# Performance work log

Hardware: AMD Instinct MI355X
Metric: run time of the kernel (lower is better)

The kernel has to match this reference:

```python
import jax, jax.numpy as jnp
import numpy as np
import math

M = 8                      # multiplicity (channels per irrep)
COMBOS = [(0,0,0),(0,1,1),(1,0,1),(1,1,0),(1,1,1),(2,1,1)]  # (edge_l, node_l, out_l)

def _cg_coeff(j1, m1, j2, m2, j3, m3):
    # standard (Racah) complex Clebsch-Gordan coefficient <j1 m1 j2 m2 | j3 m3>
    if m3 != m1 + m2:
        return 0.0
    f = math.factorial
    vmin = max(0, j2 - j3 - m1, j1 + m2 - j3)
    vmax = min(j1 + j2 - j3, j1 - m1, j2 + m2)
    pref = (2*j3 + 1) * f(j3+j1-j2) * f(j3-j1+j2) * f(j1+j2-j3) / f(j1+j2+j3+1)
    pref *= f(j3+m3) * f(j3-m3) * f(j1-m1) * f(j1+m1) * f(j2-m2) * f(j2+m2)
    s = 0.0
    for v in range(vmin, vmax + 1):
        s += (-1)**v / (f(v) * f(j1+j2-j3-v) * f(j1-m1-v) * f(j2+m2-v)
                        * f(j3-j2+m1+v) * f(j3-j1-m2+v))
    return math.sqrt(pref) * s

def _su2_cg(l1, l2, l3):
    C = np.zeros((2*l1+1, 2*l2+1, 2*l3+1), dtype=np.complex128)
    for m1 in range(-l1, l1+1):
        for m2 in range(-l2, l2+1):
            m3 = m1 + m2
            if -l3 <= m3 <= l3:
                C[m1+l1, m2+l2, m3+l3] = _cg_coeff(l1, m1, l2, m2, l3, m3)
    return C

def _qmat(l):
    # real -> complex spherical-harmonic change of basis (e3nn convention)
    q = np.zeros((2*l+1, 2*l+1), dtype=np.complex128)
    for m in range(-l, 0):
        q[l+m, l+abs(m)] = 1/np.sqrt(2)
        q[l+m, l-abs(m)] = -1j/np.sqrt(2)
    q[l, l] = 1.0
    for m in range(1, l+1):
        q[l+m, l+abs(m)] = (-1)**m / np.sqrt(2)
        q[l+m, l-abs(m)] = 1j * (-1)**m / np.sqrt(2)
    return (-1j)**l * q

def _so3_cg(l1, l2, l3):
    # real-basis CG, normalized to unit Frobenius norm (matches e3nn _so3_clebsch_gordan)
    C = np.einsum('ij,kl,mn,ikn->jlm', _qmat(l1), _qmat(l2),
                  np.conj(_qmat(l3)).T, _su2_cg(l1, l2, l3))
    assert np.abs(C.imag).max() < 1e-6
    C = C.real
    return C / np.linalg.norm(C)

CG = {c: jnp.asarray(_so3_cg(*c), dtype=jnp.float32) for c in COMBOS}


def setup_inputs() -> dict:
    N, E = 100000, 1600000
    ks = jax.random.split(jax.random.key(0), 6)
    return {
        'node_irreps': jax.random.normal(ks[0], (N, 4*M), jnp.float32),
        'edge_index': jax.random.randint(ks[1], (2, E), 0, N, dtype=jnp.int32),
        'sh0': jax.random.normal(ks[2], (E, 1), jnp.float32),
        'sh1': jax.random.normal(ks[3], (E, 3), jnp.float32),
        'sh2': jax.random.normal(ks[4], (E, 5), jnp.float32),
        'W': jax.random.normal(ks[5], (len(COMBOS), M, M), jnp.float32),
    }


def reference(node_irreps, edge_index, sh0, sh1, sh2, W):
    N, E = node_irreps.shape[0], edge_index.shape[1]
    src = node_irreps[edge_index[0]]                    # gather: [E, 4M]
    feats = {0: src[:, :M][:, :, None],                 # scalar channels [E, M, 1]
             1: src[:, M:].reshape(E, M, 3)}            # vector channels [E, M, 3]
    sh = {0: sh0, 1: sh1, 2: sh2}
    msg = {0: jnp.zeros((E, M, 1), node_irreps.dtype),
           1: jnp.zeros((E, M, 3), node_irreps.dtype)}
    for idx, (le, ln, lo) in enumerate(COMBOS):
        # per-edge CG tensor product: [de,dn,do] x [E,de] x [E,M,dn] -> [E,M,do]
        base = jnp.einsum('ijk,ei,emj->emk', CG[(le, ln, lo)], sh[le], feats[ln])
        # channel-mixing scalar weights (in_channel -> out_channel)
        msg[lo] = msg[lo] + jnp.einsum('io,eik->eok', W[idx], base)
    tgt = edge_index[1]
    agg0 = jax.ops.segment_sum(msg[0].reshape(E, M), tgt, num_segments=N)     # [N, M]
    agg1 = jax.ops.segment_sum(msg[1].reshape(E, 3*M), tgt, num_segments=N)   # [N, 3M]
    return jnp.concatenate([agg0, agg1], axis=1)
```

## Files before the change

kernel.cpp:

```cpp
#include <hip/hip_runtime.h>

#define THREADS 256

typedef float v4f __attribute__((ext_vector_type(4)));


__global__ __launch_bounds__(THREADS) void k_hist(const int* __restrict__ tgt,
                                                  int* __restrict__ cnt, int E) {
    int e = blockIdx.x * THREADS + threadIdx.x;
    if (e < E) atomicAdd(&cnt[tgt[e]], 1);
}

__global__ __launch_bounds__(THREADS) void k_scan_partial(const int* __restrict__ cnt,
                                                          int* __restrict__ bsum, int N) {
    __shared__ int lds[THREADS];
    int base = blockIdx.x * 1024 + threadIdx.x * 4;
    int s = 0;
    #pragma unroll
    for (int k = 0; k < 4; ++k) { int i = base + k; if (i < N) s += cnt[i]; }
    lds[threadIdx.x] = s; __syncthreads();
    for (int off = THREADS / 2; off > 0; off >>= 1) {
        if (threadIdx.x < off) lds[threadIdx.x] += lds[threadIdx.x + off];
        __syncthreads();
    }
    if (threadIdx.x == 0) bsum[blockIdx.x] = lds[0];
}

__global__ __launch_bounds__(1024) void k_scan_bsum(int* __restrict__ bsum, int NB) {
    __shared__ int lds[1024];
    int t = threadIdx.x;
    int v = (t < NB) ? bsum[t] : 0;
    lds[t] = v; __syncthreads();
    for (int off = 1; off < 1024; off <<= 1) {
        int x = (t >= off) ? lds[t - off] : 0;
        __syncthreads();
        lds[t] += x;
        __syncthreads();
    }
    if (t < NB) bsum[t] = lds[t] - v;
}

__global__ __launch_bounds__(THREADS) void k_scan_final(int* __restrict__ cnt,
                                                        const int* __restrict__ bsum,
                                                        int* __restrict__ rowptr,
                                                        int N, int E) {
    __shared__ int lds[THREADS];
    int base = blockIdx.x * 1024 + threadIdx.x * 4;
    int v[4]; int local = 0;
    #pragma unroll
    for (int k = 0; k < 4; ++k) {
        int i = base + k;
        v[k] = (i < N) ? cnt[i] : 0;
        local += v[k];
    }
    lds[threadIdx.x] = local; __syncthreads();
    for (int off = 1; off < THREADS; off <<= 1) {
        int x = (threadIdx.x >= off) ? lds[threadIdx.x - off] : 0;
        __syncthreads();
        lds[threadIdx.x] += x;
        __syncthreads();
    }
    int p = lds[threadIdx.x] - local + bsum[blockIdx.x];
    #pragma unroll
    for (int k = 0; k < 4; ++k) {
        int i = base + k;
        if (i < N) { rowptr[i] = p; cnt[i] = p; p += v[k]; }
    }
    if (blockIdx.x == 0 && threadIdx.x == 0) rowptr[N] = E;
}


__global__ __launch_bounds__(THREADS) void k_scatter3(const int* __restrict__ eidx,
                                                      int* __restrict__ cursor,
                                                      const float* __restrict__ sh0,
                                                      const float* __restrict__ sh1,
                                                      const float* __restrict__ sh2,
                                                      float* __restrict__ pay,
                                                      int E) {
    int e = blockIdx.x * THREADS + threadIdx.x;
    if (e >= E) return;

    constexpr float IS10 = 0.31622776601683794f;
    constexpr float IS30 = 0.18257418583505536f;

    const int src = eidx[e];
    const int tgt = eidx[E + e];
    const int pos = atomicAdd(&cursor[tgt], 1);

    const float s  = __builtin_nontemporal_load(&sh0[e]);
    const float u0 = __builtin_nontemporal_load(&sh1[3*e+0]);
    const float u1 = __builtin_nontemporal_load(&sh1[3*e+1]);
    const float u2 = __builtin_nontemporal_load(&sh1[3*e+2]);
    const float q0 = __builtin_nontemporal_load(&sh2[5*e+0]);
    const float q1 = __builtin_nontemporal_load(&sh2[5*e+1]);
    const float q2 = __builtin_nontemporal_load(&sh2[5*e+2]);
    const float q3 = __builtin_nontemporal_load(&sh2[5*e+3]);
    const float q4 = __builtin_nontemporal_load(&sh2[5*e+4]);

    const float Q00 = -q2*IS30 - q4*IS10;
    const float Q01 =  q1*IS10;
    const float Q02 =  q0*IS10;
    const float Q11 =  2.0f*q2*IS30;
    const float Q12 =  q3*IS10;
    const float Q22 = -q2*IS30 + q4*IS10;

    float4* pr = (float4*)(pay + (size_t)pos * 16);
    pr[0] = make_float4(s, u0, u1, u2);
    pr[1] = make_float4(Q00, Q01, Q02, Q11);
    pr[2] = make_float4(Q12, Q22, __int_as_float(src), 0.f);
    pr[3] = make_float4(0.f, 0.f, 0.f, 0.f);
}


#define ACC_STRIDE 15

__global__ __launch_bounds__(THREADS) void k_agg6(const float* __restrict__ node,
                                                  const int*   __restrict__ rowptr,
                                                  const float* __restrict__ pay,
                                                  const float* __restrict__ W,
                                                  float*       __restrict__ out, int N) {
    __shared__ float sW[384];
    __shared__ float sAcc[32 * 8 * ACC_STRIDE];
    for (int t = threadIdx.x; t < 384; t += THREADS) sW[t] = W[t];
    __syncthreads();

    constexpr float IS3  = 0.57735026918962576f;
    constexpr float IS6  = 0.40824829046386302f;

    const int nodeSlot = threadIdx.x >> 3;
    const int i        = threadIdx.x & 7;
    const int n        = blockIdx.x * 32 + nodeSlot;

    float a[14];
    #pragma unroll
    for (int k = 0; k < 14; ++k) a[k] = 0.f;

    if (n < N) {
        const int jbeg = rowptr[n];
        const int jend = rowptr[n + 1];

        if (jbeg < jend) {
            const int jlast = jend - 1;

            const v4f* p0 = (const v4f*)(pay + (size_t)jbeg * 16);
            v4f c0 = __builtin_nontemporal_load(p0 + 0);
            v4f c1 = __builtin_nontemporal_load(p0 + 1);
            v4f c2 = __builtin_nontemporal_load(p0 + 2);
            const int s0 = __float_as_int(c2[2]);
            const float* nr0 = node + (size_t)s0 * 32;
            float f0 = nr0[i];
            float x  = nr0[8 + 3*i + 0];
            float y  = nr0[8 + 3*i + 1];
            float z  = nr0[8 + 3*i + 2];

            const int j1 = (jbeg + 1 < jend) ? jbeg + 1 : jlast;
            const v4f* p1 = (const v4f*)(pay + (size_t)j1 * 16);
            v4f d0 = __builtin_nontemporal_load(p1 + 0);
            v4f d1 = __builtin_nontemporal_load(p1 + 1);
            v4f d2 = __builtin_nontemporal_load(p1 + 2);

            for (int j = jbeg; j < jend; ++j) {
                const int sn = __float_as_int(d2[2]);
                const float* nrn = node + (size_t)sn * 32;
                const float nf0 = nrn[i];
                const float nx  = nrn[8 + 3*i + 0];
                const float ny  = nrn[8 + 3*i + 1];
                const float nz  = nrn[8 + 3*i + 2];
                const int j2 = (j + 2 < jend) ? j + 2 : jlast;
                const v4f* p2 = (const v4f*)(pay + (size_t)j2 * 16);
                const v4f e0 = __builtin_nontemporal_load(p2 + 0);
                const v4f e1 = __builtin_nontemporal_load(p2 + 1);
                const v4f e2 = __builtin_nontemporal_load(p2 + 2);

                const float s  = c0[0], u0 = c0[1], u1 = c0[2], u2 = c0[3];
                const float Q00 = c1[0], Q01 = c1[1], Q02 = c1[2], Q11 = c1[3];
                const float Q12 = c2[0], Q22 = c2[1];

                a[0]  += s * f0;
                a[1]  += u0*x + u1*y + u2*z;
                a[2]  += s * x;
                a[3]  += s * y;
                a[4]  += s * z;
                a[5]  += f0 * u0;
                a[6]  += f0 * u1;
                a[7]  += f0 * u2;
                a[8]  += u1*z - u2*y;
                a[9]  += u2*x - u0*z;
                a[10] += u0*y - u1*x;
                a[11] += Q00*x + Q01*y + Q02*z;
                a[12] += Q01*x + Q11*y + Q12*z;
                a[13] += Q02*x + Q12*y + Q22*z;

                c0 = d0; c1 = d1; c2 = d2;
                d0 = e0; d1 = e1; d2 = e2;
                f0 = nf0; x = nx; y = ny; z = nz;
            }
        }
    }

    #pragma unroll
    for (int k = 1; k < 8; ++k) a[k] *= IS3;
    #pragma unroll
    for (int k = 8; k < 11; ++k) a[k] *= IS6;

    float* myAcc = &sAcc[(nodeSlot * 8 + i) * ACC_STRIDE];
    #pragma unroll
    for (int k = 0; k < 14; ++k) myAcc[k] = a[k];
    __syncthreads();

    if (n < N) {
        const int o = i;
        float o0 = 0.f, ox = 0.f, oy = 0.f, oz = 0.f;
        #pragma unroll
        for (int ii = 0; ii < 8; ++ii) {
            const float* A = &sAcc[(nodeSlot * 8 + ii) * ACC_STRIDE];
            const float w0 = sW[  0 + ii*8 + o];
            const float w1 = sW[ 64 + ii*8 + o];
            const float w2 = sW[128 + ii*8 + o];
            const float w3 = sW[192 + ii*8 + o];
            const float w4 = sW[256 + ii*8 + o];
            const float w5 = sW[320 + ii*8 + o];
            o0 += w0*A[0]  + w3*A[1];
            ox += w1*A[2]  + w2*A[5] + w4*A[8]  + w5*A[11];
            oy += w1*A[3]  + w2*A[6] + w4*A[9]  + w5*A[12];
            oz += w1*A[4]  + w2*A[7] + w4*A[10] + w5*A[13];
        }
        float* orow = out + (size_t)n * 32;
        orow[o]         = o0;
        orow[8 + 3*o+0] = ox;
        orow[8 + 3*o+1] = oy;
        orow[8 + 3*o+2] = oz;
    }
}


__global__ __launch_bounds__(THREADS) void msg_kernel_atomic(
    const float* __restrict__ node,
    const int*   __restrict__ eidx,
    const float* __restrict__ sh0,
    const float* __restrict__ sh1,
    const float* __restrict__ sh2,
    const float* __restrict__ W,
    float*       __restrict__ out,
    int E)
{
    __shared__ float sW[384];
    for (int t = threadIdx.x; t < 384; t += THREADS) sW[t] = W[t];
    __syncthreads();

    int e = blockIdx.x * THREADS + threadIdx.x;
    if (e >= E) return;

    constexpr float IS3  = 0.57735026918962576f;
    constexpr float IS6  = 0.40824829046386302f;
    constexpr float IS10 = 0.31622776601683794f;
    constexpr float IS30 = 0.18257418583505536f;

    const int src = eidx[e];
    const int tgt = eidx[E + e];

    const float s  = sh0[e];
    const float u0 = sh1[3*e+0], u1 = sh1[3*e+1], u2 = sh1[3*e+2];
    const float q0 = sh2[5*e+0], q1 = sh2[5*e+1], q2 = sh2[5*e+2],
                q3 = sh2[5*e+3], q4 = sh2[5*e+4];

    const float Q00 = -q2*IS30 - q4*IS10;
    const float Q01 =  q1*IS10;
    const float Q02 =  q0*IS10;
    const float Q11 =  2.0f*q2*IS30;
    const float Q12 =  q3*IS10;
    const float Q22 = -q2*IS30 + q4*IS10;

    float f[32];
    {
        const float4* nr = (const float4*)(node + (size_t)src * 32);
        #pragma unroll
        for (int i = 0; i < 8; ++i) {
            float4 v = nr[i];
            f[4*i+0]=v.x; f[4*i+1]=v.y; f[4*i+2]=v.z; f[4*i+3]=v.w;
        }
    }

    float msg[32];
    #pragma unroll
    for (int j = 0; j < 32; ++j) msg[j] = 0.0f;

    const float s13 = s * IS3;

    #pragma unroll
    for (int i = 0; i < 8; ++i) {
        const float f0i = f[i];
        const float x = f[8+3*i+0], y = f[8+3*i+1], z = f[8+3*i+2];
        const float c0  = s * f0i;
        const float c3  = IS3 * (u0*x + u1*y + u2*z);
        const float p2  = IS3 * f0i;
        const float c1x = s13*x, c1y = s13*y, c1z = s13*z;
        const float c2x = p2*u0, c2y = p2*u1, c2z = p2*u2;
        const float c4x = IS6*(u1*z - u2*y);
        const float c4y = IS6*(u2*x - u0*z);
        const float c4z = IS6*(u0*y - u1*x);
        const float c5x = Q00*x + Q01*y + Q02*z;
        const float c5y = Q01*x + Q11*y + Q12*z;
        const float c5z = Q02*x + Q12*y + Q22*z;

        float wr[6][8];
        #pragma unroll
        for (int c = 0; c < 6; ++c) {
            float4 aa = *(const float4*)&sW[c*64 + i*8 + 0];
            float4 bb = *(const float4*)&sW[c*64 + i*8 + 4];
            wr[c][0]=aa.x; wr[c][1]=aa.y; wr[c][2]=aa.z; wr[c][3]=aa.w;
            wr[c][4]=bb.x; wr[c][5]=bb.y; wr[c][6]=bb.z; wr[c][7]=bb.w;
        }

        #pragma unroll
        for (int o = 0; o < 8; ++o) {
            msg[o] += wr[0][o]*c0 + wr[3][o]*c3;
            msg[8+3*o+0] += wr[1][o]*c1x + wr[2][o]*c2x + wr[4][o]*c4x + wr[5][o]*c5x;
            msg[8+3*o+1] += wr[1][o]*c1y + wr[2][o]*c2y + wr[4][o]*c4y + wr[5][o]*c5y;
            msg[8+3*o+2] += wr[1][o]*c1z + wr[2][o]*c2z + wr[4][o]*c4z + wr[5][o]*c5z;
        }
    }

    float* orow = out + (size_t)tgt * 32;
    #pragma unroll
    for (int j = 0; j < 32; ++j) unsafeAtomicAdd(orow + j, msg[j]);
}


extern "C" void kernel_launch(void* const* d_in, const int* in_sizes, int n_in,
                              void* d_out, int out_size, void* d_ws, size_t ws_size,
                              hipStream_t stream) {
    const float* node = (const float*)d_in[0];
    const int*   eidx = (const int*)d_in[1];
    const float* sh0  = (const float*)d_in[2];
    const float* sh1  = (const float*)d_in[3];
    const float* sh2  = (const float*)d_in[4];
    const float* W    = (const float*)d_in[5];
    float* out = (float*)d_out;

    const int E = in_sizes[2];
    const int N = in_sizes[0] / 32;
    const int NB = (N + 1023) / 1024;

    size_t int_words = (size_t)(N + 1) + N + 1024;
    size_t pay_off_w = (int_words + 15) & ~(size_t)15;
    size_t need      = (pay_off_w + (size_t)E * 16) * sizeof(float);

    const int gridE = (E + THREADS - 1) / THREADS;

    if (ws_size >= need && NB <= 1024) {
        int* rowptr = (int*)d_ws;
        int* cnt    = rowptr + (N + 1);
        int* bsum   = cnt + N;
        float* pay  = (float*)d_ws + pay_off_w;

        hipMemsetAsync(cnt, 0, (size_t)N * sizeof(int), stream);

        k_hist<<<gridE, THREADS, 0, stream>>>(eidx + E, cnt, E);
        k_scan_partial<<<NB, THREADS, 0, stream>>>(cnt, bsum, N);
        k_scan_bsum<<<1, 1024, 0, stream>>>(bsum, NB);
        k_scan_final<<<NB, THREADS, 0, stream>>>(cnt, bsum, rowptr, N, E);

        k_scatter3<<<gridE, THREADS, 0, stream>>>(eidx, cnt, sh0, sh1, sh2, pay, E);

        k_agg6<<<(N + 31) / 32, THREADS, 0, stream>>>(node, rowptr, pay, W, out, N);
    } else {
        hipMemsetAsync(d_out, 0, (size_t)out_size * sizeof(float), stream);
        msg_kernel_atomic<<<gridE, THREADS, 0, stream>>>(
            node, eidx, sh0, sh1, sh2, W, out, E);
    }
}
```

Measured before the change: 360.8 us.

## Parallelize edges across lanes in aggregation, precompute edge ranks, transpose node features

The aggregation kernel now gives each wavefront 8 nodes processed one at a time. Within a node, the 8 lane groups each take a different edge of a chunk of 8, and the partial sums are reduced with cross-lane shuffles. Before, each thread walked a node's whole edge list serially. The histogram pass now records each edge's rank within its target, so the scatter pass computes the CSR position directly instead of doing a second atomic. A new transpose kernel repacks node features so each lane's (scalar, x, y, z) is one contiguous 16-byte load. These add workspace use and an extra kernel, plus shuffle reduction work per node.

Result: slower. 375.1 us (+3.9%).

```diff
diff --git a/kernel.cpp b/kernel.cpp
--- a/kernel.cpp
+++ b/kernel.cpp
@@ -4,6 +4,13 @@
 
 typedef float v4f __attribute__((ext_vector_type(4)));
 
+
+__global__ __launch_bounds__(THREADS) void k_hist2(const int* __restrict__ tgt,
+                                                   int* __restrict__ cnt,
+                                                   int* __restrict__ ke, int E) {
+    int e = blockIdx.x * THREADS + threadIdx.x;
+    if (e < E) ke[e] = atomicAdd(&cnt[tgt[e]], 1);
+}
 
 __global__ __launch_bounds__(THREADS) void k_hist(const int* __restrict__ tgt,
                                                   int* __restrict__ cnt, int E) {
@@ -70,7 +77,24 @@
 }
 
 
-__global__ __launch_bounds__(THREADS) void k_scatter3(const int* __restrict__ eidx,
+__global__ __launch_bounds__(THREADS) void k_ntrans(const float* __restrict__ node,
+                                                    float* __restrict__ nodeT, int NT8) {
+    int t = blockIdx.x * THREADS + threadIdx.x;
+    if (t >= NT8) return;
+    int n = t >> 3, i = t & 7;
+    const float* nr = node + (size_t)n * 32;
+    v4f v;
+    v[0] = nr[i];
+    v[1] = nr[8 + 3*i + 0];
+    v[2] = nr[8 + 3*i + 1];
+    v[3] = nr[8 + 3*i + 2];
+    *(v4f*)(nodeT + (size_t)t * 4) = v;
+}
+
+
+__global__ __launch_bounds__(THREADS) void k_scatter4(const int* __restrict__ eidx,
+                                                      const int* __restrict__ ke,
+                                                      const int* __restrict__ rowptr,
                                                       int* __restrict__ cursor,
                                                       const float* __restrict__ sh0,
                                                       const float* __restrict__ sh1,
@@ -85,7 +109,9 @@
 
     const int src = eidx[e];
     const int tgt = eidx[E + e];
-    const int pos = atomicAdd(&cursor[tgt], 1);
+    int pos;
+    if (ke) pos = rowptr[tgt] + ke[e];
+    else    pos = atomicAdd(&cursor[tgt], 1);
 
     const float s  = __builtin_nontemporal_load(&sh0[e]);
     const float u0 = __builtin_nontemporal_load(&sh1[3*e+0]);
@@ -114,122 +140,155 @@
 
 #define ACC_STRIDE 15
 
-__global__ __launch_bounds__(THREADS) void k_agg6(const float* __restrict__ node,
+__global__ __launch_bounds__(THREADS) void k_agg7(const float* __restrict__ node,
+                                                  const float* __restrict__ nodeT,
                                                   const int*   __restrict__ rowptr,
                                                   const float* __restrict__ pay,
                                                   const float* __restrict__ W,
-                                                  float*       __restrict__ out, int N) {
+                                                  float*       __restrict__ out,
+                                                  int N, int useT) {
     __shared__ float sW[384];
     __shared__ float sAcc[32 * 8 * ACC_STRIDE];
     for (int t = threadIdx.x; t < 384; t += THREADS) sW[t] = W[t];
     __syncthreads();
 
-    constexpr float IS3  = 0.57735026918962576f;
-    constexpr float IS6  = 0.40824829046386302f;
-
-    const int nodeSlot = threadIdx.x >> 3;
-    const int i        = threadIdx.x & 7;
-    const int n        = blockIdx.x * 32 + nodeSlot;
-
-    float a[14];
-    #pragma unroll
-    for (int k = 0; k < 14; ++k) a[k] = 0.f;
-
-    if (n < N) {
-        const int jbeg = rowptr[n];
-        const int jend = rowptr[n + 1];
-
-        if (jbeg < jend) {
-            const int jlast = jend - 1;
-
-            const v4f* p0 = (const v4f*)(pay + (size_t)jbeg * 16);
-            v4f c0 = __builtin_nontemporal_load(p0 + 0);
-            v4f c1 = __builtin_nontemporal_load(p0 + 1);
-            v4f c2 = __builtin_nontemporal_load(p0 + 2);
-            const int s0 = __float_as_int(c2[2]);
-            const float* nr0 = node + (size_t)s0 * 32;
-            float f0 = nr0[i];
-            float x  = nr0[8 + 3*i + 0];
-            float y  = nr0[8 + 3*i + 1];
-            float z  = nr0[8 + 3*i + 2];
-
-            const int j1 = (jbeg + 1 < jend) ? jbeg + 1 : jlast;
-            const v4f* p1 = (const v4f*)(pay + (size_t)j1 * 16);
-            v4f d0 = __builtin_nontemporal_load(p1 + 0);
-            v4f d1 = __builtin_nontemporal_load(p1 + 1);
-            v4f d2 = __builtin_nontemporal_load(p1 + 2);
-
-            for (int j = jbeg; j < jend; ++j) {
-                const int sn = __float_as_int(d2[2]);
-                const float* nrn = node + (size_t)sn * 32;
-                const float nf0 = nrn[i];
-                const float nx  = nrn[8 + 3*i + 0];
-                const float ny  = nrn[8 + 3*i + 1];
-                const float nz  = nrn[8 + 3*i + 2];
-                const int j2 = (j + 2 < jend) ? j + 2 : jlast;
-                const v4f* p2 = (const v4f*)(pay + (size_t)j2 * 16);
-                const v4f e0 = __builtin_nontemporal_load(p2 + 0);
-                const v4f e1 = __builtin_nontemporal_load(p2 + 1);
-                const v4f e2 = __builtin_nontemporal_load(p2 + 2);
-
-                const float s  = c0[0], u0 = c0[1], u1 = c0[2], u2 = c0[3];
-                const float Q00 = c1[0], Q01 = c1[1], Q02 = c1[2], Q11 = c1[3];
-                const float Q12 = c2[0], Q22 = c2[1];
-
-                a[0]  += s * f0;
-                a[1]  += u0*x + u1*y + u2*z;
-                a[2]  += s * x;
-                a[3]  += s * y;
-                a[4]  += s * z;
-                a[5]  += f0 * u0;
-                a[6]  += f0 * u1;
-                a[7]  += f0 * u2;
-                a[8]  += u1*z - u2*y;
-                a[9]  += u2*x - u0*z;
-                a[10] += u0*y - u1*x;
-                a[11] += Q00*x + Q01*y + Q02*z;
-                a[12] += Q01*x + Q11*y + Q12*z;
-                a[13] += Q02*x + Q12*y + Q22*z;
-
-                c0 = d0; c1 = d1; c2 = d2;
-                d0 = e0; d1 = e1; d2 = e2;
-                f0 = nf0; x = nx; y = ny; z = nz;
+    constexpr float IS3 = 0.57735026918962576f;
+    constexpr float IS6 = 0.40824829046386302f;
+
+    const int lane  = threadIdx.x & 63;
+    const int wv    = threadIdx.x >> 6;
+    const int i     = lane & 7;
+    const int jslot = lane >> 3;
+    const int nbase = blockIdx.x * 32 + wv * 8;
+
+    for (int t = 0; t < 8; ++t) {
+        const int n = nbase + t;
+
+        float a[14];
+        #pragma unroll
+        for (int k = 0; k < 14; ++k) a[k] = 0.f;
+
+        if (n < N) {
+            const int jbeg = rowptr[n];
+            const int jend = rowptr[n + 1];
+
+            if (jbeg < jend) {
+                int j  = jbeg + jslot;
+                int jc = (j < jend) ? j : (jend - 1);
+                float mcur = (j < jend) ? 1.f : 0.f;
+                const v4f* p = (const v4f*)(pay + (size_t)jc * 16);
+                v4f c0 = p[0], c1 = p[1], c2 = p[2];
+                int src = __float_as_int(c2[2]);
+                v4f nf;
+                if (useT) {
+                    nf = *(const v4f*)(nodeT + ((size_t)src * 8 + i) * 4);
+                } else {
+                    const float* nr = node + (size_t)src * 32;
+                    nf[0] = nr[i];
+                    nf[1] = nr[8 + 3*i + 0];
+                    nf[2] = nr[8 + 3*i + 1];
+                    nf[3] = nr[8 + 3*i + 2];
+                }
+
+                for (int g0 = jbeg; g0 < jend; g0 += 8) {
+                    const int gn = g0 + 8;
+                    const bool more = gn < jend;
+                    v4f d0, d1, d2; float mnext = 0.f;
+                    if (more) {
+                        int jn  = gn + jslot;
+                        int jnc = (jn < jend) ? jn : (jend - 1);
+                        mnext = (jn < jend) ? 1.f : 0.f;
+                        const v4f* pn = (const v4f*)(pay + (size_t)jnc * 16);
+                        d0 = pn[0]; d1 = pn[1]; d2 = pn[2];
+                    }
+
+                    const float f0 = nf[0] * mcur;
+                    const float x  = nf[1] * mcur;
+                    const float y  = nf[2] * mcur;
+                    const float z  = nf[3] * mcur;
+                    const float s   = c0[0], u0 = c0[1], u1 = c0[2], u2 = c0[3];
+                    const float Q00 = c1[0], Q01 = c1[1], Q02 = c1[2], Q11 = c1[3];
+                    const float Q12 = c2[0], Q22 = c2[1];
+
+                    a[0]  += s * f0;
+                    a[1]  += u0*x + u1*y + u2*z;
+                    a[2]  += s * x;
+                    a[3]  += s * y;
+                    a[4]  += s * z;
+                    a[5]  += f0 * u0;
+                    a[6]  += f0 * u1;
+                    a[7]  += f0 * u2;
+                    a[8]  += u1*z - u2*y;
+                    a[9]  += u2*x - u0*z;
+                    a[10] += u0*y - u1*x;
+                    a[11] += Q00*x + Q01*y + Q02*z;
+                    a[12] += Q01*x + Q11*y + Q12*z;
+                    a[13] += Q02*x + Q12*y + Q22*z;
+
+                    if (more) {
+                        int srcn = __float_as_int(d2[2]);
+                        if (useT) {
+                            nf = *(const v4f*)(nodeT + ((size_t)srcn * 8 + i) * 4);
+                        } else {
+                            const float* nrn = node + (size_t)srcn * 32;
+                            nf[0] = nrn[i];
+                            nf[1] = nrn[8 + 3*i + 0];
+                            nf[2] = nrn[8 + 3*i + 1];
+                            nf[3] = nrn[8 + 3*i + 2];
+                        }
+                        c0 = d0; c1 = d1; c2 = d2; mcur = mnext;
+                    }
+                }
             }
         }
-    }
-
-    #pragma unroll
-    for (int k = 1; k < 8; ++k) a[k] *= IS3;
-    #pragma unroll
-    for (int k = 8; k < 11; ++k) a[k] *= IS6;
-
-    float* myAcc = &sAcc[(nodeSlot * 8 + i) * ACC_STRIDE];
-    #pragma unroll
-    for (int k = 0; k < 14; ++k) myAcc[k] = a[k];
+
+        #pragma unroll
+        for (int k = 0; k < 14; ++k) {
+            float v = a[k];
+            v += __shfl_xor(v, 8);
+            v += __shfl_xor(v, 16);
+            v += __shfl_xor(v, 32);
+            a[k] = v;
+        }
+
+        if (n < N && jslot == 0) {
+            #pragma unroll
+            for (int k = 1; k < 8; ++k) a[k] *= IS3;
+            #pragma unroll
+            for (int k = 8; k < 11; ++k) a[k] *= IS6;
+            float* myAcc = &sAcc[((wv * 8 + t) * 8 + i) * ACC_STRIDE];
+            #pragma unroll
+            for (int k = 0; k < 14; ++k) myAcc[k] = a[k];
+        }
+    }
     __syncthreads();
 
-    if (n < N) {
-        const int o = i;
-        float o0 = 0.f, ox = 0.f, oy = 0.f, oz = 0.f;
-        #pragma unroll
-        for (int ii = 0; ii < 8; ++ii) {
-            const float* A = &sAcc[(nodeSlot * 8 + ii) * ACC_STRIDE];
-            const float w0 = sW[  0 + ii*8 + o];
-            const float w1 = sW[ 64 + ii*8 + o];
-            const float w2 = sW[128 + ii*8 + o];
-            const float w3 = sW[192 + ii*8 + o];
-            const float w4 = sW[256 + ii*8 + o];
-            const float w5 = sW[320 + ii*8 + o];
-            o0 += w0*A[0]  + w3*A[1];
-            ox += w1*A[2]  + w2*A[5] + w4*A[8]  + w5*A[11];
-            oy += w1*A[3]  + w2*A[6] + w4*A[9]  + w5*A[12];
-            oz += w1*A[4]  + w2*A[7] + w4*A[10] + w5*A[13];
-        }
-        float* orow = out + (size_t)n * 32;
-        orow[o]         = o0;
-        orow[8 + 3*o+0] = ox;
-        orow[8 + 3*o+1] = oy;
-        orow[8 + 3*o+2] = oz;
+    {
+        const int nodeSlot = threadIdx.x >> 3;
+        const int o        = threadIdx.x & 7;
+        const int n        = blockIdx.x * 32 + nodeSlot;
+        if (n < N) {
+            float o0 = 0.f, ox = 0.f, oy = 0.f, oz = 0.f;
+            #pragma unroll
+            for (int ii = 0; ii < 8; ++ii) {
+                const float* A = &sAcc[(nodeSlot * 8 + ii) * ACC_STRIDE];
+                const float w0 = sW[  0 + ii*8 + o];
+                const float w1 = sW[ 64 + ii*8 + o];
+                const float w2 = sW[128 + ii*8 + o];
+                const float w3 = sW[192 + ii*8 + o];
+                const float w4 = sW[256 + ii*8 + o];
+                const float w5 = sW[320 + ii*8 + o];
+                o0 += w0*A[0]  + w3*A[1];
+                ox += w1*A[2]  + w2*A[5] + w4*A[8]  + w5*A[11];
+                oy += w1*A[3]  + w2*A[6] + w4*A[9]  + w5*A[12];
+                oz += w1*A[4]  + w2*A[7] + w4*A[10] + w5*A[13];
+            }
+            float* orow = out + (size_t)n * 32;
+            orow[o]         = o0;
+            orow[8 + 3*o+0] = ox;
+            orow[8 + 3*o+1] = oy;
+            orow[8 + 3*o+2] = oz;
+        }
     }
 }
 
@@ -342,28 +401,48 @@
     const int N = in_sizes[0] / 32;
     const int NB = (N + 1023) / 1024;
 
-    size_t int_words = (size_t)(N + 1) + N + 1024;
-    size_t pay_off_w = (int_words + 15) & ~(size_t)15;
-    size_t need      = (pay_off_w + (size_t)E * 16) * sizeof(float);
+    size_t base_w = (size_t)(N + 1) + N + 1024;
+    size_t int12  = base_w + (size_t)E;
+    size_t pay12  = (int12 + 15) & ~(size_t)15;
+    size_t nT1    = pay12 + (size_t)E * 16;
+    size_t need1  = (nT1 + (size_t)N * 32) * sizeof(float);
+    size_t need2  = (pay12 + (size_t)E * 16) * sizeof(float);
+    size_t pay3   = (base_w + 15) & ~(size_t)15;
+    size_t need3  = (pay3 + (size_t)E * 16) * sizeof(float);
 
     const int gridE = (E + THREADS - 1) / THREADS;
 
-    if (ws_size >= need && NB <= 1024) {
-        int* rowptr = (int*)d_ws;
+    if (ws_size >= need3 && NB <= 1024) {
+        const bool useKe = (ws_size >= need2);
+        const bool useT  = (ws_size >= need1);
+
+        int* wsI    = (int*)d_ws;
+        int* rowptr = wsI;
         int* cnt    = rowptr + (N + 1);
         int* bsum   = cnt + N;
-        float* pay  = (float*)d_ws + pay_off_w;
+        int* ke     = useKe ? (bsum + 1024) : nullptr;
+        float* pay  = (float*)d_ws + (useKe ? pay12 : pay3);
+        float* nodeT = useT ? ((float*)d_ws + nT1) : nullptr;
 
         hipMemsetAsync(cnt, 0, (size_t)N * sizeof(int), stream);
 
-        k_hist<<<gridE, THREADS, 0, stream>>>(eidx + E, cnt, E);
+        if (useKe)
+            k_hist2<<<gridE, THREADS, 0, stream>>>(eidx + E, cnt, ke, E);
+        else
+            k_hist<<<gridE, THREADS, 0, stream>>>(eidx + E, cnt, E);
+
+        if (useT)
+            k_ntrans<<<(8 * N + THREADS - 1) / THREADS, THREADS, 0, stream>>>(node, nodeT, 8 * N);
+
         k_scan_partial<<<NB, THREADS, 0, stream>>>(cnt, bsum, N);
         k_scan_bsum<<<1, 1024, 0, stream>>>(bsum, NB);
         k_scan_final<<<NB, THREADS, 0, stream>>>(cnt, bsum, rowptr, N, E);
 
-        k_scatter3<<<gridE, THREADS, 0, stream>>>(eidx, cnt, sh0, sh1, sh2, pay, E);
-
-        k_agg6<<<(N + 31) / 32, THREADS, 0, stream>>>(node, rowptr, pay, W, out, N);
+        k_scatter4<<<gridE, THREADS, 0, stream>>>(eidx, ke, rowptr, cnt,
+                                                  sh0, sh1, sh2, pay, E);
+
+        k_agg7<<<(N + 31) / 32, THREADS, 0, stream>>>(node, nodeT, rowptr, pay, W,
+                                                      out, N, useT ? 1 : 0);
     } else {
         hipMemsetAsync(d_out, 0, (size_t)out_size * sizeof(float), stream);
         msg_kernel_atomic<<<gridE, THREADS, 0, stream>>>(
```
